# Optimization experiments

Measured on AMD Instinct MI355X. Metric: run time of the kernel, lower is better.

## Reference

```python
import jax, jax.numpy as jnp
import numpy as np

LN_ZERO = -99.0            # log(~0) sentinel used by the original repo's clamp_min/set_invalid_positions
F, E, V = 1_000_000, 3_000_000, 500_000   # factors, edges (= 3*F), variables
S, L = 2, 3                # n_var_states, max_clause_length
DAMP_FV, DAMP_VF = 0.9, 0.9


def setup_inputs() -> dict:
    key = jax.random.key(0)
    k1, k2, k3 = jax.random.split(key, 3)
    rng = np.random.default_rng(0)
    pos = (np.arange(E) % L).astype(np.int64)            # slot of each edge within its factor
    adj0 = np.repeat(np.arange(F, dtype=np.int32), L)    # factor id of each edge
    adj1 = rng.integers(0, V, size=E).astype(np.int32)   # variable id of each edge
    cfg = np.indices((S, S, S))                          # [3,2,2,2]: state of slot p at each config
    # factor->var scatter-logsumexp bins: (edge, config) -> edge*S + state of edge's slot
    fvi = (np.arange(E, dtype=np.int64)[:, None, None, None] * S + cfg[pos]).reshape(-1).astype(np.int32)
    # var->factor permutation: flat (e,s,a,b) -> flat (e,c0,c1,c2) with c[slot]=s, rest = (a,b) in order
    s_g, a_g, b_g = cfg
    dest = np.stack([s_g * 4 + a_g * 2 + b_g,
                     a_g * 4 + s_g * 2 + b_g,
                     a_g * 4 + b_g * 2 + s_g])           # [3,2,2,2]
    ivf = (np.arange(E, dtype=np.int64)[:, None, None, None] * (S ** L) + dest[pos]).reshape(-1).astype(np.int32)
    return {
        "var_factor_prev_msg": jax.random.normal(k1, (E, S), jnp.float32),
        "factor_var_prev_msg": jax.random.normal(k2, (E, S), jnp.float32),
        "factor_prev_marginals": jax.random.normal(k3, (F, S, S, S), jnp.float32),
        "factor_var_adjacency": jnp.asarray(np.stack([adj0, adj1])),
        "factor_var_indices": jnp.asarray(fvi),
        "indexes_var_factor": jnp.asarray(ivf),
        "factor_valid_configs": jnp.zeros((F, S, S, S), jnp.int32),  # 0 == valid config
    }


def _segment_logsumexp(src, idx, n):
    m = jax.ops.segment_max(src, idx, num_segments=n)
    m = jax.lax.stop_gradient(jnp.where(jnp.isfinite(m), m, 0.0))
    s = jax.ops.segment_sum(jnp.exp(src - m[idx]), idx, num_segments=n)
    return m + jnp.log(s)


def _lse_keep0(x):
    # log_sum_exp over all dims except 0, keepdims (original log_sum_exp(dim_to_keep=[0]))
    return jax.nn.logsumexp(x.reshape(x.shape[0], -1), axis=1).reshape((x.shape[0],) + (1,) * (x.ndim - 1))


def reference(var_factor_prev_msg, factor_var_prev_msg, factor_prev_marginals,
              factor_var_adjacency, factor_var_indices, indexes_var_factor,
              factor_valid_configs):
    adj0, adj1 = factor_var_adjacency[0], factor_var_adjacency[1]
    valid = factor_valid_configs == 0
    # ---- factor -> var messages (compute_factor_var_msg) ----
    fpm = jnp.where(valid, factor_prev_marginals, LN_ZERO)          # set_invalid_positions
    arranged = jnp.where(valid[adj0], fpm[adj0], LN_ZERO)           # [E,S,S,S] gather per edge
    lse = _segment_logsumexp(arranged.reshape(-1), factor_var_indices, E * S)
    fv_msg = jnp.maximum(lse.reshape(E, S) - var_factor_prev_msg, LN_ZERO)
    fv_msg = jnp.maximum(DAMP_FV * fv_msg + (1.0 - DAMP_FV) * factor_var_prev_msg, LN_ZERO)
    # ---- variable marginals: scatter_add over edge->var, then logsumexp normalize ----
    var_marg = jax.ops.segment_sum(fv_msg, adj1, num_segments=V)    # [V,S]
    var_marg = var_marg - _lse_keep0(var_marg)
    # ---- var -> factor messages (compute_var_factor_msg: marginal minus incoming, damped) ----
    vf_msg = jnp.maximum(var_marg[adj1] - fv_msg, LN_ZERO)
    vf_msg = jnp.maximum(DAMP_VF * vf_msg + (1.0 - DAMP_VF) * var_factor_prev_msg, LN_ZERO)
    # ---- expand to factor-config space and permutation-scatter (indexes_var_factor) ----
    full = jnp.broadcast_to(vf_msg[:, :, None, None], (E, S, S, S)).reshape(-1)
    arranged_vf = jnp.zeros(E * S ** L, vf_msg.dtype).at[indexes_var_factor].add(full)
    arranged_vf = arranged_vf.reshape(E, S, S, S)
    arranged_vf = arranged_vf - _lse_keep0(arranged_vf)
    # ---- factor marginals: scatter_add over edge->factor, normalize, mask invalid ----
    fac_marg = jax.ops.segment_sum(arranged_vf, adj0, num_segments=F)
    fac_marg = fac_marg - _lse_keep0(fac_marg)
    fac_marg = jnp.where(valid, fac_marg, LN_ZERO)
    return vf_msg, fv_msg, var_marg, fac_marg
```

## Files before the change

### kernel.cpp

```cpp
#include <hip/hip_runtime.h>


#define LN_ZERO (-99.0f)
#define F_CNT 1000000
#define E_CNT 3000000
#define V_CNT 500000
#define DAMP 0.9f
#define ONE_MINUS_DAMP 0.1f

__device__ __forceinline__ float lse4(float a, float b, float c, float d) {
    float m = fmaxf(fmaxf(a, b), fmaxf(c, d));
    float s = expf(a - m) + expf(b - m) + expf(c - m) + expf(d - m);
    return m + logf(s);
}

__global__ __launch_bounds__(256, 4) void k1a_stream(
    const float* __restrict__ vfpm,
    const float* __restrict__ fvpm,
    const float* __restrict__ fpm,
    float*       __restrict__ out_fv,
    float*       __restrict__ var_marg)
{
    int e = blockIdx.x * blockDim.x + threadIdx.x;
    if (e >= E_CNT) return;
    if (e < 2 * V_CNT) var_marg[e] = 0.0f;

    int f = e / 3;
    int p = e - 3 * f;

    const float4* fp4 = reinterpret_cast<const float4*>(fpm);
    float4 lo = fp4[2 * f];
    float4 hi = fp4[2 * f + 1];
    float x0 = lo.x, x1 = lo.y, x2 = lo.z, x3 = lo.w;
    float x4 = hi.x, x5 = hi.y, x6 = hi.z, x7 = hi.w;

    bool p0 = (p == 0), p1 = (p == 1), p2 = (p == 2);
    float a0 = x0;
    float a1 = p2 ? x2 : x1;
    float a2 = p0 ? x2 : x4;
    float a3 = p0 ? x3 : (p1 ? x5 : x6);
    float b0 = p0 ? x4 : (p1 ? x2 : x1);
    float b1 = p0 ? x5 : x3;
    float b2 = p2 ? x5 : x6;
    float b3 = x7;
    float lse0 = lse4(a0, a1, a2, a3);
    float lse1 = lse4(b0, b1, b2, b3);

    float2 vp = reinterpret_cast<const float2*>(vfpm)[e];
    float2 pv = reinterpret_cast<const float2*>(fvpm)[e];

    float m0 = fmaxf(lse0 - vp.x, LN_ZERO);
    float m1 = fmaxf(lse1 - vp.y, LN_ZERO);
    m0 = fmaxf(DAMP * m0 + ONE_MINUS_DAMP * pv.x, LN_ZERO);
    m1 = fmaxf(DAMP * m1 + ONE_MINUS_DAMP * pv.y, LN_ZERO);
    reinterpret_cast<float2*>(out_fv)[e] = make_float2(m0, m1);
}

__global__ __launch_bounds__(256, 8) void k1b_scatter(
    const float* __restrict__ fv,
    const int*   __restrict__ adj1,
    float*       __restrict__ var_marg)
{
    int e = blockIdx.x * blockDim.x + threadIdx.x;
    if (e >= E_CNT) return;
    float2 m = reinterpret_cast<const float2*>(fv)[e];
    int v = adj1[e];
    atomicAdd(&var_marg[2 * v], m.x);
    atomicAdd(&var_marg[2 * v + 1], m.y);
}

__global__ __launch_bounds__(256, 4) void k_norm_var(float* __restrict__ vm) {
    int v = blockIdx.x * blockDim.x + threadIdx.x;
    if (v >= V_CNT) return;
    float2* vm2 = reinterpret_cast<float2*>(vm);
    float2 x = vm2[v];
    float m = fmaxf(x.x, x.y);
    float l = m + logf(expf(x.x - m) + expf(x.y - m));
    vm2[v] = make_float2(x.x - l, x.y - l);
}

#define K3_FPB 84
__global__ __launch_bounds__(256, 4) void k_var_factor(
    const float* __restrict__ vfpm,
    const float* __restrict__ fv,
    const float* __restrict__ var_marg,
    const int*   __restrict__ adj1,
    float*       __restrict__ out_vf,
    float*       __restrict__ out_fm)
{
    __shared__ float2 sA[256];
    __shared__ float  sFM[K3_FPB * 9];

    int fb = blockIdx.x * K3_FPB;
    int tid = threadIdx.x;
    int e = 3 * fb + tid;

    if (tid < 3 * K3_FPB && e < E_CNT) {
        const float2* vf2 = reinterpret_cast<const float2*>(vfpm);
        const float2* fv2 = reinterpret_cast<const float2*>(fv);
        const float2* vm2 = reinterpret_cast<const float2*>(var_marg);
        float2 f2 = fv2[e];
        float2 pp = vf2[e];
        float2 vm = vm2[adj1[e]];
        float v0 = fmaxf(vm.x - f2.x, LN_ZERO);
        float v1 = fmaxf(vm.y - f2.y, LN_ZERO);
        v0 = fmaxf(DAMP * v0 + ONE_MINUS_DAMP * pp.x, LN_ZERO);
        v1 = fmaxf(DAMP * v1 + ONE_MINUS_DAMP * pp.y, LN_ZERO);
        reinterpret_cast<float2*>(out_vf)[e] = make_float2(v0, v1);
        float m = fmaxf(v0, v1);
        float n = m + logf(4.0f * (expf(v0 - m) + expf(v1 - m)));
        sA[tid] = make_float2(v0 - n, v1 - n);
    }
    __syncthreads();

    if (tid < K3_FPB && (fb + tid) < F_CNT) {
        float2 A0 = sA[3 * tid];
        float2 A1 = sA[3 * tid + 1];
        float2 A2 = sA[3 * tid + 2];
        float a[3][2] = {{A0.x, A0.y}, {A1.x, A1.y}, {A2.x, A2.y}};
        float g[8];
#pragma unroll
        for (int c = 0; c < 8; ++c)
            g[c] = a[0][(c >> 2) & 1] + a[1][(c >> 1) & 1] + a[2][c & 1];
        float m8 = g[0];
#pragma unroll
        for (int c = 1; c < 8; ++c) m8 = fmaxf(m8, g[c]);
        float s = 0.0f;
#pragma unroll
        for (int c = 0; c < 8; ++c) s += expf(g[c] - m8);
        float L = m8 + logf(s);
#pragma unroll
        for (int c = 0; c < 8; ++c) sFM[9 * tid + c] = g[c] - L;
    }
    __syncthreads();

    if (tid < 2 * K3_FPB && (fb + (tid >> 1)) < F_CNT) {
        int base = 9 * (tid >> 1) + 4 * (tid & 1);
        float4 v = make_float4(sFM[base], sFM[base + 1], sFM[base + 2], sFM[base + 3]);
        reinterpret_cast<float4*>(out_fm)[2 * fb + tid] = v;
    }
}

extern "C" void kernel_launch(void* const* d_in, const int* in_sizes, int n_in,
                              void* d_out, int out_size, void* d_ws, size_t ws_size,
                              hipStream_t stream) {
    const float* vfpm = (const float*)d_in[0];
    const float* fvpm = (const float*)d_in[1];
    const float* fpm  = (const float*)d_in[2];
    const int*   adj  = (const int*)d_in[3];
    const int*   adj1 = adj + E_CNT;

    float* out    = (float*)d_out;
    float* out_vf = out;
    float* out_fv = out + (size_t)E_CNT * 2;
    float* out_vm = out + (size_t)E_CNT * 4;
    float* out_fm = out_vm + (size_t)V_CNT * 2;

    const int BLK = 256;
    k1a_stream<<<(E_CNT + BLK - 1) / BLK, BLK, 0, stream>>>(
        vfpm, fvpm, fpm, out_fv, out_vm);
    k1b_scatter<<<(E_CNT + BLK - 1) / BLK, BLK, 0, stream>>>(
        out_fv, adj1, out_vm);
    k_norm_var<<<(V_CNT + BLK - 1) / BLK, BLK, 0, stream>>>(out_vm);
    k_var_factor<<<(F_CNT + K3_FPB - 1) / K3_FPB, BLK, 0, stream>>>(
        vfpm, out_fv, out_vm, adj1, out_vf, out_fm);
}
```

Before: 577.5 us.

## Fuse factor-to-var message computation with var-marginal scatter, share per-factor LSE

Merges the streaming factor-to-variable message kernel and the atomic scatter kernel into one block-per-84-factors kernel. Each factor's six marginal log-sum-exps are computed once in shared memory and reused by its three edges, instead of each edge re-reading the factor and doing two LSEs. The atomics now use register values, so the fv buffer is not re-read and one launch is dropped. The zero-init of var_marg moves to a memset, and only 252 of 256 threads do edge work.

Measured after the change: 554.4 us. 1.04x faster.

```diff
diff --git a/kernel.cpp b/kernel.cpp
--- a/kernel.cpp
+++ b/kernel.cpp
@@ -14,59 +14,55 @@
     return m + logf(s);
 }
 
-__global__ __launch_bounds__(256, 4) void k1a_stream(
+#define K1_FPB 84
+__global__ __launch_bounds__(256, 4) void k_factor_var(
     const float* __restrict__ vfpm,
     const float* __restrict__ fvpm,
     const float* __restrict__ fpm,
+    const int*   __restrict__ adj1,
     float*       __restrict__ out_fv,
     float*       __restrict__ var_marg)
 {
-    int e = blockIdx.x * blockDim.x + threadIdx.x;
-    if (e >= E_CNT) return;
-    if (e < 2 * V_CNT) var_marg[e] = 0.0f;
+    __shared__ float sLse[K1_FPB][6];
 
-    int f = e / 3;
-    int p = e - 3 * f;
+    int fb = blockIdx.x * K1_FPB;
+    int tid = threadIdx.x;
 
-    const float4* fp4 = reinterpret_cast<const float4*>(fpm);
-    float4 lo = fp4[2 * f];
-    float4 hi = fp4[2 * f + 1];
-    float x0 = lo.x, x1 = lo.y, x2 = lo.z, x3 = lo.w;
-    float x4 = hi.x, x5 = hi.y, x6 = hi.z, x7 = hi.w;
+    if (tid < K1_FPB && (fb + tid) < F_CNT) {
+        int f = fb + tid;
+        const float4* fp4 = reinterpret_cast<const float4*>(fpm);
+        float4 lo = fp4[2 * f];
+        float4 hi = fp4[2 * f + 1];
+        float x0 = lo.x, x1 = lo.y, x2 = lo.z, x3 = lo.w;
+        float x4 = hi.x, x5 = hi.y, x6 = hi.z, x7 = hi.w;
+        sLse[tid][0] = lse4(x0, x1, x2, x3);
+        sLse[tid][1] = lse4(x4, x5, x6, x7);
+        sLse[tid][2] = lse4(x0, x1, x4, x5);
+        sLse[tid][3] = lse4(x2, x3, x6, x7);
+        sLse[tid][4] = lse4(x0, x2, x4, x6);
+        sLse[tid][5] = lse4(x1, x3, x5, x7);
+    }
+    __syncthreads();
 
-    bool p0 = (p == 0), p1 = (p == 1), p2 = (p == 2);
-    float a0 = x0;
-    float a1 = p2 ? x2 : x1;
-    float a2 = p0 ? x2 : x4;
-    float a3 = p0 ? x3 : (p1 ? x5 : x6);
-    float b0 = p0 ? x4 : (p1 ? x2 : x1);
-    float b1 = p0 ? x5 : x3;
-    float b2 = p2 ? x5 : x6;
-    float b3 = x7;
-    float lse0 = lse4(a0, a1, a2, a3);
-    float lse1 = lse4(b0, b1, b2, b3);
+    int e = 3 * fb + tid;
+    if (tid < 3 * K1_FPB && e < E_CNT) {
+        int lf = tid / 3;
+        int p  = tid - 3 * lf;
+        float l0 = sLse[lf][2 * p];
+        float l1 = sLse[lf][2 * p + 1];
 
-    float2 vp = reinterpret_cast<const float2*>(vfpm)[e];
-    float2 pv = reinterpret_cast<const float2*>(fvpm)[e];
+        float2 vp = reinterpret_cast<const float2*>(vfpm)[e];
+        float2 pv = reinterpret_cast<const float2*>(fvpm)[e];
+        float m0 = fmaxf(l0 - vp.x, LN_ZERO);
+        float m1 = fmaxf(l1 - vp.y, LN_ZERO);
+        m0 = fmaxf(DAMP * m0 + ONE_MINUS_DAMP * pv.x, LN_ZERO);
+        m1 = fmaxf(DAMP * m1 + ONE_MINUS_DAMP * pv.y, LN_ZERO);
+        reinterpret_cast<float2*>(out_fv)[e] = make_float2(m0, m1);
 
-    float m0 = fmaxf(lse0 - vp.x, LN_ZERO);
-    float m1 = fmaxf(lse1 - vp.y, LN_ZERO);
-    m0 = fmaxf(DAMP * m0 + ONE_MINUS_DAMP * pv.x, LN_ZERO);
-    m1 = fmaxf(DAMP * m1 + ONE_MINUS_DAMP * pv.y, LN_ZERO);
-    reinterpret_cast<float2*>(out_fv)[e] = make_float2(m0, m1);
-}
-
-__global__ __launch_bounds__(256, 8) void k1b_scatter(
-    const float* __restrict__ fv,
-    const int*   __restrict__ adj1,
-    float*       __restrict__ var_marg)
-{
-    int e = blockIdx.x * blockDim.x + threadIdx.x;
-    if (e >= E_CNT) return;
-    float2 m = reinterpret_cast<const float2*>(fv)[e];
-    int v = adj1[e];
-    atomicAdd(&var_marg[2 * v], m.x);
-    atomicAdd(&var_marg[2 * v + 1], m.y);
+        int v = adj1[e];
+        atomicAdd(&var_marg[2 * v], m0);
+        atomicAdd(&var_marg[2 * v + 1], m1);
+    }
 }
 
 __global__ __launch_bounds__(256, 4) void k_norm_var(float* __restrict__ vm) {
@@ -156,11 +152,11 @@
     float* out_vm = out + (size_t)E_CNT * 4;
     float* out_fm = out_vm + (size_t)V_CNT * 2;
 
+    hipMemsetAsync(out_vm, 0, (size_t)V_CNT * 2 * sizeof(float), stream);
+
     const int BLK = 256;
-    k1a_stream<<<(E_CNT + BLK - 1) / BLK, BLK, 0, stream>>>(
-        vfpm, fvpm, fpm, out_fv, out_vm);
-    k1b_scatter<<<(E_CNT + BLK - 1) / BLK, BLK, 0, stream>>>(
-        out_fv, adj1, out_vm);
+    k_factor_var<<<(F_CNT + K1_FPB - 1) / K1_FPB, BLK, 0, stream>>>(
+        vfpm, fvpm, fpm, adj1, out_fv, out_vm);
     k_norm_var<<<(V_CNT + BLK - 1) / BLK, BLK, 0, stream>>>(out_vm);
     k_var_factor<<<(F_CNT + K3_FPB - 1) / K3_FPB, BLK, 0, stream>>>(
         vfpm, out_fv, out_vm, adj1, out_vf, out_fm);
```
